# Kernel tuning notes

Measured on AMD Instinct MI355X. Metric: run time of the kernel, lower is better.

The kernel has to match this reference:

```python
import jax, jax.numpy as jnp
import numpy as np

EPS = 1e-6      # zero-token detection eps
LN_EPS = 1e-5   # torch LayerNorm default
H = 8           # num_heads


def setup_inputs() -> dict:
    key = jax.random.key(0)
    ks = jax.random.split(key, 6)
    B, T, D = 4, 2048, 512
    embs = jax.random.normal(ks[0], (B, T, D), jnp.float32)
    labels = jax.random.uniform(ks[1], (B, T), jnp.float32)
    s = 1.0 / np.sqrt(D)
    ln_g = jnp.ones((D,), jnp.float32)
    ln_b = jnp.zeros((D,), jnp.float32)
    in_proj_w = jax.random.uniform(ks[2], (3 * D, D), jnp.float32, -s, s)
    in_proj_b = jnp.zeros((3 * D,), jnp.float32)
    out_w = jax.random.uniform(ks[3], (D, D), jnp.float32, -s, s)
    out_b = jnp.zeros((D,), jnp.float32)
    alpha = jnp.float32(1.0)
    beta = jnp.float32(0.0)
    return {"embs": embs, "labels": labels, "ln_g": ln_g, "ln_b": ln_b,
            "in_proj_w": in_proj_w, "in_proj_b": in_proj_b,
            "out_w": out_w, "out_b": out_b, "alpha": alpha, "beta": beta}


def reference(embs, labels, ln_g, ln_b, in_proj_w, in_proj_b, out_w, out_b, alpha, beta):
    B, T, D = embs.shape
    h, dh = H, D // H
    # pre-LayerNorm
    mu = embs.mean(-1, keepdims=True)
    var = ((embs - mu) ** 2).mean(-1, keepdims=True)
    x = (embs - mu) / jnp.sqrt(var + LN_EPS) * ln_g + ln_b
    # key padding mask from all-zero tokens (computed on normalized x, as in source)
    kpm = jnp.abs(x).sum(-1) <= EPS                      # [B,T] bool
    w = jnp.where(kpm, jnp.float32(0.0), labels)         # zero labels on masked tokens
    # fused qkv projection (nn.MultiheadAttention in_proj)
    qkv = x @ in_proj_w.T + in_proj_b                    # [B,T,3D]
    q, k, v = jnp.split(qkv, 3, axis=-1)
    def sp(a):
        return a.reshape(B, T, h, dh).transpose(0, 2, 1, 3)  # [B,h,T,dh]
    q, k, v = sp(q), sp(k), sp(v)
    scores = jnp.einsum('bhqd,bhkd->bhqk', q, k) / np.sqrt(dh)
    # additive label bias: alpha * labels (broadcast over heads & queries) + beta
    scores = scores + (alpha * w[:, None, None, :] + beta)
    # key padding mask -> -inf (use large negative for stability)
    scores = jnp.where(kpm[:, None, None, :], jnp.float32(-1e30), scores)
    a = jax.nn.softmax(scores, axis=-1)
    o = jnp.einsum('bhqk,bhkd->bhqd', a, v).transpose(0, 2, 1, 3).reshape(B, T, D)
    o = o @ out_w.T + out_b
    o = jnp.nan_to_num(o, nan=0.0, posinf=0.0, neginf=0.0)
    # masked mean pool over T
    m = (~kpm)[..., None].astype(o.dtype)                # [B,T,1]
    pooled = (o * m).sum(1) / jnp.maximum(m.sum(1), 1.0)  # [B,D]
    return pooled
```

## Files before the change

kernel.cpp:

```cpp
#include <hip/hip_runtime.h>
#include <math.h>

#define T 2048
#define D 512
#define NH 8
#define DH 64
#define NB 4
#define NTOK (NB * T)
#define LOG2E 1.44269504f
#define QSCALE (0.125f * LOG2E)

using bf16x8 = __attribute__((ext_vector_type(8))) short;
using f32x4  = __attribute__((ext_vector_type(4))) float;

static __device__ __forceinline__ unsigned short f2bf(float f) {
    union { float f; unsigned u; } v; v.f = f;
    unsigned r = v.u + 0x7fffu + ((v.u >> 16) & 1u);
    return (unsigned short)(r >> 16);
}
#if __has_builtin(__builtin_amdgcn_cvt_pk_bf16_f32)
static __device__ __forceinline__ unsigned pack_bf16_pair(float a, float b) {
    auto r = __builtin_amdgcn_cvt_pk_bf16_f32(a, b);
    union { decltype(r) v; unsigned u; } c; c.v = r;
    return c.u;
}
#else
static __device__ __forceinline__ unsigned pack_bf16_pair(float a, float b) {
    union { float f; unsigned u; } ua, ub; ua.f = a; ub.f = b;
    unsigned ra = ua.u + 0x7fffu + ((ua.u >> 16) & 1u);
    unsigned rb = ub.u + 0x7fffu + ((ub.u >> 16) & 1u);
    return __builtin_amdgcn_perm(rb, ra, 0x07060302);
}
#endif


__global__ __launch_bounds__(256) void ln_kernel(
    const float* __restrict__ embs, const float* __restrict__ labels,
    const float* __restrict__ g, const float* __restrict__ bb,
    const float* __restrict__ alpha_p, const float* __restrict__ beta_p,
    unsigned short* __restrict__ xfrag, float* __restrict__ wexp,
    float* __restrict__ kpmf)
{
    __shared__ __align__(16) unsigned short Xs[16][520];
    int tid = threadIdx.x, wave = tid >> 6, lane = tid & 63;
    int quad = lane >> 4, lm = lane & 15;
    int t16 = blockIdx.x;

    float4 g0 = *(const float4*)(g + lane * 8), g1 = *(const float4*)(g + lane * 8 + 4);
    float4 c0 = *(const float4*)(bb + lane * 8), c1 = *(const float4*)(bb + lane * 8 + 4);
    float gv[8] = {g0.x, g0.y, g0.z, g0.w, g1.x, g1.y, g1.z, g1.w};
    float cv[8] = {c0.x, c0.y, c0.z, c0.w, c1.x, c1.y, c1.z, c1.w};

    for (int tt = 0; tt < 4; ++tt) {
        int n = t16 * 16 + wave * 4 + tt;
        const float* e = embs + (size_t)n * D + lane * 8;
        float4 a4 = *(const float4*)e, b4 = *(const float4*)(e + 4);
        float v[8] = {a4.x, a4.y, a4.z, a4.w, b4.x, b4.y, b4.z, b4.w};

        float s = 0.f, ss = 0.f;
        #pragma unroll
        for (int j = 0; j < 8; ++j) { s += v[j]; ss += v[j] * v[j]; }
        #pragma unroll
        for (int o = 1; o <= 32; o <<= 1) {
            s += __shfl_xor(s, o, 64);
            ss += __shfl_xor(ss, o, 64);
        }
        float mu = s * (1.0f / D);
        float var = ss * (1.0f / D) - mu * mu;
        float rstd = rsqrtf(var + 1e-5f);

        float x[8], as = 0.f;
        #pragma unroll
        for (int j = 0; j < 8; ++j) {
            x[j] = (v[j] - mu) * rstd * gv[j] + cv[j];
            as += fabsf(x[j]);
        }
        uint4 pk;
        pk.x = pack_bf16_pair(x[0], x[1]);
        pk.y = pack_bf16_pair(x[2], x[3]);
        pk.z = pack_bf16_pair(x[4], x[5]);
        pk.w = pack_bf16_pair(x[6], x[7]);
        *(uint4*)&Xs[wave * 4 + tt][lane * 8] = pk;

        #pragma unroll
        for (int o = 1; o <= 32; o <<= 1) as += __shfl_xor(as, o, 64);
        if (lane == 0) {
            int kpm = (as <= 1e-6f);
            kpmf[n] = kpm ? 1.0f : 0.0f;
            wexp[n] = kpm ? 0.0f : __expf(alpha_p[0] * labels[n] + beta_p[0]);
        }
    }
    __syncthreads();
    #pragma unroll
    for (int i = 0; i < 4; ++i) {
        int kc = wave * 4 + i;
        bf16x8 fr = *(const bf16x8*)&Xs[lm][kc * 32 + quad * 8];
        *(bf16x8*)(xfrag + ((size_t)(t16 * 16 + kc) * 64 + lane) * 8) = fr;
    }
}

__global__ __launch_bounds__(256) void wconv_kernel(
    const float* __restrict__ w, unsigned short* __restrict__ wbfrag)
{
    __shared__ __align__(16) unsigned short Ws[16][520];
    int tid = threadIdx.x, wave = tid >> 6, lane = tid & 63;
    int quad = lane >> 4, lm = lane & 15;
    int j16 = blockIdx.x;

    for (int tt = 0; tt < 4; ++tt) {
        int j = j16 * 16 + wave * 4 + tt;
        const float* wp = w + (size_t)j * D + lane * 8;
        float4 a4 = *(const float4*)wp, b4 = *(const float4*)(wp + 4);
        uint4 pk;
        pk.x = pack_bf16_pair(a4.x, a4.y);
        pk.y = pack_bf16_pair(a4.z, a4.w);
        pk.z = pack_bf16_pair(b4.x, b4.y);
        pk.w = pack_bf16_pair(b4.z, b4.w);
        *(uint4*)&Ws[wave * 4 + tt][lane * 8] = pk;
    }
    __syncthreads();
    #pragma unroll
    for (int i = 0; i < 4; ++i) {
        int kc = wave * 4 + i;
        bf16x8 fr = *(const bf16x8*)&Ws[lm][kc * 32 + quad * 8];
        *(bf16x8*)(wbfrag + ((size_t)(j16 * 16 + kc) * 64 + lane) * 8) = fr;
    }
}

__global__ __launch_bounds__(256) void wfrag_fill(
    const float* __restrict__ wexp, unsigned short* __restrict__ vfrag)
{
    int idx = blockIdx.x * 256 + threadIdx.x;
    int lane = idx & 63, chunk = idx >> 6;
    int kk = chunk & 1, t64 = (chunk >> 1) & 31, bh = chunk >> 6;
    int lm = lane & 15, quad = lane >> 4;
    int b_ = bh >> 3;
    size_t base = (((size_t)chunk * 5 + 4) * 64 + lane) * 8;
    if (lm == 0) {
        int key0 = t64 * 64 + kk * 32 + quad * 8;
        const float* wp = wexp + b_ * T + key0;
        unsigned short vv[8];
        #pragma unroll
        for (int e = 0; e < 8; ++e) vv[e] = f2bf(wp[e]);
        *(uint4*)(vfrag + base) = *(uint4*)vv;
    } else {
        uint4 z = {0u, 0u, 0u, 0u};
        *(uint4*)(vfrag + base) = z;
    }
}

__global__ __launch_bounds__(256) void qkv_mfma(
    const unsigned short* __restrict__ xfrag, const unsigned short* __restrict__ wbfrag,
    const float* __restrict__ bias, const float* __restrict__ wexp,
    unsigned short* __restrict__ qfrag, unsigned short* __restrict__ kfrag,
    unsigned short* __restrict__ vfrag)
{
    __shared__ __align__(16) unsigned short Ls[4][64][72];
    int tid = threadIdx.x;
    int wave = tid >> 6, lane = tid & 63, quad = lane >> 4, lm = lane & 15;
    int wr = wave >> 1, wc = wave & 1;
    int m0 = blockIdx.x * 128 + wr * 64;
    int j0 = blockIdx.y * 128 + wc * 64;
    int mt16 = m0 >> 4, jt16 = j0 >> 4;

    f32x4 acc[4][4];
    #pragma unroll
    for (int a = 0; a < 4; ++a)
        #pragma unroll
        for (int b = 0; b < 4; ++b) acc[a][b] = (f32x4){0.f,0.f,0.f,0.f};

    bf16x8 af0[4], bf0[4], af1[4], bf1[4];
    auto load_ab = [&](int kc, bf16x8 (&af)[4], bf16x8 (&bf)[4]) {
        #pragma unroll
        for (int mf = 0; mf < 4; ++mf)
            af[mf] = *(const bf16x8*)(xfrag + ((size_t)((mt16 + mf) * 16 + kc) * 64 + lane) * 8);
        #pragma unroll
        for (int nt = 0; nt < 4; ++nt)
            bf[nt] = *(const bf16x8*)(wbfrag + ((size_t)((jt16 + nt) * 16 + kc) * 64 + lane) * 8);
    };
    auto do_mfma = [&](bf16x8 (&af)[4], bf16x8 (&bf)[4]) {
        #pragma unroll
        for (int mf = 0; mf < 4; ++mf)
            #pragma unroll
            for (int nt = 0; nt < 4; ++nt)
                acc[mf][nt] = __builtin_amdgcn_mfma_f32_16x16x32_bf16(af[mf], bf[nt], acc[mf][nt], 0, 0, 0);
    };

    load_ab(0, af0, bf0);
    for (int kc = 0; kc < 16; kc += 2) {
        load_ab(kc + 1, af1, bf1);
        do_mfma(af0, bf0);
        load_ab((kc + 2) & 15, af0, bf0);
        do_mfma(af1, bf1);
    }

    int part = j0 >> 9;
    int h = (j0 & 511) >> 6;
    int b_ = m0 >> 11, tloc = m0 & (T - 1);
    int bh = b_ * NH + h;
    float bcol[4];
    #pragma unroll
    for (int nt = 0; nt < 4; ++nt) bcol[nt] = bias[j0 + nt * 16 + lm];

    if (part == 2) {
        float wv[4][4];
        #pragma unroll
        for (int mf = 0; mf < 4; ++mf)
            #pragma unroll
            for (int r = 0; r < 4; ++r)
                wv[mf][r] = wexp[b_ * T + tloc + mf * 16 + quad * 4 + r];
        #pragma unroll
        for (int mf = 0; mf < 4; ++mf)
            #pragma unroll
            for (int nt = 0; nt < 4; ++nt) {
                uint2 pw;
                pw.x = pack_bf16_pair((acc[mf][nt][0] + bcol[nt]) * wv[mf][0],
                                      (acc[mf][nt][1] + bcol[nt]) * wv[mf][1]);
                pw.y = pack_bf16_pair((acc[mf][nt][2] + bcol[nt]) * wv[mf][2],
                                      (acc[mf][nt][3] + bcol[nt]) * wv[mf][3]);
                *(uint2*)&Ls[wave][nt * 16 + lm][mf * 16 + quad * 4] = pw;
            }
        #pragma unroll
        for (int nt = 0; nt < 4; ++nt)
            #pragma unroll
            for (int kk = 0; kk < 2; ++kk) {
                bf16x8 fr = *(const bf16x8*)&Ls[wave][nt * 16 + lm][kk * 32 + quad * 8];
                size_t chunk = ((((size_t)bh * 32 + (tloc >> 6)) * 2 + kk) * 5) + nt;
                *(bf16x8*)(vfrag + chunk * 512 + lane * 8) = fr;
            }
    } else {
        float scale = (part == 0) ? QSCALE : 1.0f;
        #pragma unroll
        for (int mf = 0; mf < 4; ++mf)
            #pragma unroll
            for (int nt = 0; nt < 4; ++nt)
                #pragma unroll
                for (int r = 0; r < 4; ++r)
                    Ls[wave][mf * 16 + quad * 4 + r][nt * 16 + lm] =
                        f2bf((acc[mf][nt][r] + bcol[nt]) * scale);
        if (part == 0) {
            #pragma unroll
            for (int mf = 0; mf < 4; ++mf)
                #pragma unroll
                for (int kk = 0; kk < 2; ++kk) {
                    bf16x8 fr = *(const bf16x8*)&Ls[wave][mf * 16 + lm][kk * 32 + quad * 8];
                    size_t chunk = ((size_t)bh * 128 + (tloc >> 4) + mf) * 2 + kk;
                    *(bf16x8*)(qfrag + chunk * 512 + lane * 8) = fr;
                }
        } else {
            #pragma unroll
            for (int nta = 0; nta < 4; ++nta)
                #pragma unroll
                for (int kk = 0; kk < 2; ++kk) {
                    bf16x8 fr = *(const bf16x8*)&Ls[wave][lm * 4 + nta][kk * 32 + quad * 8];
                    size_t chunk = ((((size_t)bh * 32 + (tloc >> 6)) * 2 + kk) * 4) + nta;
                    *(bf16x8*)(kfrag + chunk * 512 + lane * 8) = fr;
                }
        }
    }
}

__global__ __launch_bounds__(256, 2) void attn_mfma(
    const unsigned short* __restrict__ qfrag, const unsigned short* __restrict__ kfrag,
    const unsigned short* __restrict__ vfrag, const float* __restrict__ kpmf,
    float* __restrict__ S)
{
    __shared__ __align__(16) unsigned short Ps[4][64][72];
    __shared__ float Lx[2][2][64];
    int g = blockIdx.x;
    int bh = g & 31, q0 = (g >> 5) * 128;
    int tid = threadIdx.x, wave = tid >> 6, lane = tid & 63;
    int quad = lane >> 4, lm = lane & 15;
    int qh = wave >> 1, ks = wave & 1;
    int qbase = q0 + qh * 64;
    int b_ = bh >> 3, h = bh & 7;

    bf16x8 qf[4][2];
    int t16b = (qbase >> 4);
    #pragma unroll
    for (int mf = 0; mf < 4; ++mf)
        #pragma unroll
        for (int kk = 0; kk < 2; ++kk)
            qf[mf][kk] = *(const bf16x8*)(qfrag +
                (((size_t)(bh * 128 + t16b + mf) * 2 + kk) * 64 + lane) * 8);

    f32x4 accO[4][4], accL[4];
    #pragma unroll
    for (int mf = 0; mf < 4; ++mf) {
        #pragma unroll
        for (int nt = 0; nt < 4; ++nt) accO[mf][nt] = (f32x4){0.f,0.f,0.f,0.f};
        accL[mf] = (f32x4){0.f,0.f,0.f,0.f};
    }

    const unsigned short* kb = kfrag + (size_t)bh * 32 * 8 * 512 + (size_t)lane * 8;
    const unsigned short* vb = vfrag + (size_t)bh * 32 * 10 * 512 + (size_t)lane * 8;
    int t0k = ks * 16;

    bf16x8 kf0[4][2], kf1[4][2];
    auto load_k = [&](int t64, bf16x8 (&kf)[4][2]) {
        const unsigned short* p = kb + (size_t)t64 * 8 * 512;
        #pragma unroll
        for (int kk = 0; kk < 2; ++kk)
            #pragma unroll
            for (int nt = 0; nt < 4; ++nt)
                kf[nt][kk] = *(const bf16x8*)(p + ((size_t)kk * 4 + nt) * 512);
    };

    auto process = [&](int t64, bf16x8 (&kf)[4][2]) {
        const unsigned short* p = vb + (size_t)t64 * 10 * 512;
        bf16x8 vf[5][2];
        #pragma unroll
        for (int kk = 0; kk < 2; ++kk)
            #pragma unroll
            for (int nt = 0; nt < 5; ++nt)
                vf[nt][kk] = *(const bf16x8*)(p + ((size_t)kk * 5 + nt) * 512);

        #pragma unroll
        for (int mf = 0; mf < 4; ++mf) {
            f32x4 s[4];
            #pragma unroll
            for (int nt = 0; nt < 4; ++nt) {
                f32x4 t0 = (f32x4){0.f,0.f,0.f,0.f};
                t0 = __builtin_amdgcn_mfma_f32_16x16x32_bf16(qf[mf][0], kf[nt][0], t0, 0, 0, 0);
                t0 = __builtin_amdgcn_mfma_f32_16x16x32_bf16(qf[mf][1], kf[nt][1], t0, 0, 0, 0);
                s[nt] = t0;
            }
            int rowb = mf * 16 + quad * 4;
            #pragma unroll
            for (int r = 0; r < 4; ++r) {
                float p0 = __builtin_amdgcn_exp2f(s[0][r]);
                float p1 = __builtin_amdgcn_exp2f(s[1][r]);
                float p2 = __builtin_amdgcn_exp2f(s[2][r]);
                float p3 = __builtin_amdgcn_exp2f(s[3][r]);
                uint2 pw;
                pw.x = pack_bf16_pair(p0, p1);
                pw.y = pack_bf16_pair(p2, p3);
                *(uint2*)&Ps[wave][rowb + r][lm * 4] = pw;
            }
        }

        bf16x8 pf[4][2];
        #pragma unroll
        for (int mf = 0; mf < 4; ++mf)
            #pragma unroll
            for (int kk = 0; kk < 2; ++kk)
                pf[mf][kk] = *(const bf16x8*)&Ps[wave][mf * 16 + lm][kk * 32 + quad * 8];

        #pragma unroll
        for (int mf = 0; mf < 4; ++mf) {
            #pragma unroll
            for (int nt = 0; nt < 4; ++nt) {
                accO[mf][nt] = __builtin_amdgcn_mfma_f32_16x16x32_bf16(pf[mf][0], vf[nt][0], accO[mf][nt], 0, 0, 0);
                accO[mf][nt] = __builtin_amdgcn_mfma_f32_16x16x32_bf16(pf[mf][1], vf[nt][1], accO[mf][nt], 0, 0, 0);
            }
            accL[mf] = __builtin_amdgcn_mfma_f32_16x16x32_bf16(pf[mf][0], vf[4][0], accL[mf], 0, 0, 0);
            accL[mf] = __builtin_amdgcn_mfma_f32_16x16x32_bf16(pf[mf][1], vf[4][1], accL[mf], 0, 0, 0);
        }
    };

    load_k(t0k, kf0);
    for (int i = 0; i < 16; i += 2) {
        load_k(t0k + i + 1, kf1);
        process(t0k + i, kf0);
        load_k(t0k + ((i + 2) & 15), kf0);
        process(t0k + i + 1, kf1);
    }

    if (lm == 0) {
        #pragma unroll
        for (int mf = 0; mf < 4; ++mf)
            #pragma unroll
            for (int r = 0; r < 4; ++r)
                Lx[qh][ks][mf * 16 + quad * 4 + r] = accL[mf][r];
    }
    __syncthreads();

    float pooled[4] = {0.f, 0.f, 0.f, 0.f};
    #pragma unroll
    for (int mf = 0; mf < 4; ++mf)
        #pragma unroll
        for (int r = 0; r < 4; ++r) {
            int rloc = mf * 16 + quad * 4 + r;
            float l = Lx[qh][0][rloc] + Lx[qh][1][rloc];
            float w = (1.0f - kpmf[b_ * T + qbase + rloc]) / l;
            #pragma unroll
            for (int nt = 0; nt < 4; ++nt) pooled[nt] += accO[mf][nt][r] * w;
        }
    #pragma unroll
    for (int nt = 0; nt < 4; ++nt) {
        pooled[nt] += __shfl_xor(pooled[nt], 16, 64);
        pooled[nt] += __shfl_xor(pooled[nt], 32, 64);
    }
    if (quad == 0) {
        #pragma unroll
        for (int nt = 0; nt < 4; ++nt)
            atomicAdd(&S[b_ * D + h * DH + nt * 16 + lm], pooled[nt]);
    }
}

__global__ __launch_bounds__(256) void out_kernel(
    const float* __restrict__ S, const float* __restrict__ kpmf,
    const float* __restrict__ Wo, const float* __restrict__ bo,
    float* __restrict__ out)
{
    __shared__ float Sl[512];
    __shared__ float cs[4];
    __shared__ float pr[4][64];
    int b_ = blockIdx.x >> 3;
    int cg = blockIdx.x & 7;
    int tid = threadIdx.x;
    int col = tid & 63, kq = tid >> 6;
    Sl[tid] = S[b_ * D + tid];
    Sl[tid + 256] = S[b_ * D + tid + 256];
    const float* kp = kpmf + b_ * T;
    float c = 0.f;
    for (int t = tid; t < T; t += 256) c += kp[t];
    #pragma unroll
    for (int o = 32; o; o >>= 1) c += __shfl_xor(c, o, 64);
    if ((tid & 63) == 0) cs[tid >> 6] = c;
    __syncthreads();
    float masked = cs[0] + cs[1] + cs[2] + cs[3];
    float cnt = (float)T - masked;
    float inv = 1.0f / fmaxf(cnt, 1.0f);

    int d = cg * 64 + col;
    const float4* wr4 = (const float4*)(Wo + (size_t)d * D + kq * 128);
    float dot = 0.f;
    #pragma unroll 8
    for (int i = 0; i < 32; ++i) {
        float4 w4 = wr4[i];
        int kbase = kq * 128 + i * 4;
        dot += Sl[kbase + 0] * w4.x + Sl[kbase + 1] * w4.y +
               Sl[kbase + 2] * w4.z + Sl[kbase + 3] * w4.w;
    }
    pr[kq][col] = dot;
    __syncthreads();
    if (kq == 0) {
        float tot = pr[0][col] + pr[1][col] + pr[2][col] + pr[3][col];
        out[b_ * D + d] = (tot + bo[d] * cnt) * inv;
    }
}

extern "C" void kernel_launch(void* const* d_in, const int* in_sizes, int n_in,
                              void* d_out, int out_size, void* d_ws, size_t ws_size,
                              hipStream_t stream) {
    const float* embs   = (const float*)d_in[0];
    const float* labels = (const float*)d_in[1];
    const float* ln_g   = (const float*)d_in[2];
    const float* ln_b   = (const float*)d_in[3];
    const float* ipw    = (const float*)d_in[4];
    const float* ipb    = (const float*)d_in[5];
    const float* ow     = (const float*)d_in[6];
    const float* obb    = (const float*)d_in[7];
    const float* alpha  = (const float*)d_in[8];
    const float* beta   = (const float*)d_in[9];
    float* out = (float*)d_out;

    unsigned short* xfrag  = (unsigned short*)d_ws;
    unsigned short* wbfrag = xfrag + (size_t)NTOK * D;
    unsigned short* qfrag  = wbfrag + (size_t)3 * D * D;
    unsigned short* kfrag  = qfrag + (size_t)NTOK * D;
    unsigned short* vfrag  = kfrag + (size_t)NTOK * D;
    float* wexp = (float*)(vfrag + (size_t)32 * 32 * 2 * 5 * 512);
    float* kpmf = wexp + NTOK;
    float* S    = kpmf + NTOK;

    hipMemsetAsync(S, 0, (size_t)NB * D * sizeof(float), stream);
    ln_kernel<<<NTOK / 16, 256, 0, stream>>>(embs, labels, ln_g, ln_b, alpha, beta,
                                             xfrag, wexp, kpmf);
    wconv_kernel<<<(3 * D) / 16, 256, 0, stream>>>(ipw, wbfrag);
    wfrag_fill<<<512, 256, 0, stream>>>(wexp, vfrag);
    dim3 gq(NTOK / 128, (3 * D) / 128);
    qkv_mfma<<<gq, 256, 0, stream>>>(xfrag, wbfrag, ipb, wexp, qfrag, kfrag, vfrag);
    attn_mfma<<<32 * (T / 128), 256, 0, stream>>>(qfrag, kfrag, vfrag, kpmf, S);
    out_kernel<<<NB * 8, 256, 0, stream>>>(S, kpmf, ow, obb, out);
}
```

Measured before the change: 165.3 us.

## Software-pipeline QK-exp and PV stages with double-buffered P tiles

Restructures the attention inner loop so the QK^T+exp2 stage for key tile t runs alongside the PV MFMA stage for tile t-1. P tiles now go through a double-buffered LDS array, and the K register double buffer is replaced by a single buffer that is loaded ahead. s_setprio raises wave priority around the MFMA sections so MFMA work can interleave with exp/LDS work from other waves. The goal is to hide LDS round-trip and transcendental latency behind matrix work. The cost is double the LDS for P and possible register-pressure changes, which could hurt occupancy at 2 blocks per CU.

```diff
diff --git a/kernel.cpp b/kernel.cpp
--- a/kernel.cpp
+++ b/kernel.cpp
@@ -265,7 +265,7 @@
     const unsigned short* __restrict__ vfrag, const float* __restrict__ kpmf,
     float* __restrict__ S)
 {
-    __shared__ __align__(16) unsigned short Ps[4][64][72];
+    __shared__ __align__(16) unsigned short Ps[4][2][64][72];
     __shared__ float Lx[2][2][64];
     int g = blockIdx.x;
     int bh = g & 31, q0 = (g >> 5) * 128;
@@ -296,8 +296,8 @@
     const unsigned short* vb = vfrag + (size_t)bh * 32 * 10 * 512 + (size_t)lane * 8;
     int t0k = ks * 16;
 
-    bf16x8 kf0[4][2], kf1[4][2];
-    auto load_k = [&](int t64, bf16x8 (&kf)[4][2]) {
+    bf16x8 kf[4][2];
+    auto load_k = [&](int t64) {
         const unsigned short* p = kb + (size_t)t64 * 8 * 512;
         #pragma unroll
         for (int kk = 0; kk < 2; ++kk)
@@ -305,19 +305,26 @@
             for (int nt = 0; nt < 4; ++nt)
                 kf[nt][kk] = *(const bf16x8*)(p + ((size_t)kk * 4 + nt) * 512);
     };
-
-    auto process = [&](int t64, bf16x8 (&kf)[4][2]) {
+    auto load_v = [&](int t64, bf16x8 (&vf)[5][2]) {
         const unsigned short* p = vb + (size_t)t64 * 10 * 512;
-        bf16x8 vf[5][2];
         #pragma unroll
         for (int kk = 0; kk < 2; ++kk)
             #pragma unroll
             for (int nt = 0; nt < 5; ++nt)
                 vf[nt][kk] = *(const bf16x8*)(p + ((size_t)kk * 5 + nt) * 512);
-
+    };
+    auto load_p = [&](int buf, bf16x8 (&pf)[4][2]) {
+        #pragma unroll
+        for (int mf = 0; mf < 4; ++mf)
+            #pragma unroll
+            for (int kk = 0; kk < 2; ++kk)
+                pf[mf][kk] = *(const bf16x8*)&Ps[wave][buf][mf * 16 + lm][kk * 32 + quad * 8];
+    };
+    auto qk_exp = [&](int buf) {
         #pragma unroll
         for (int mf = 0; mf < 4; ++mf) {
             f32x4 s[4];
+            __builtin_amdgcn_s_setprio(1);
             #pragma unroll
             for (int nt = 0; nt < 4; ++nt) {
                 f32x4 t0 = (f32x4){0.f,0.f,0.f,0.f};
@@ -325,6 +332,7 @@
                 t0 = __builtin_amdgcn_mfma_f32_16x16x32_bf16(qf[mf][1], kf[nt][1], t0, 0, 0, 0);
                 s[nt] = t0;
             }
+            __builtin_amdgcn_s_setprio(0);
             int rowb = mf * 16 + quad * 4;
             #pragma unroll
             for (int r = 0; r < 4; ++r) {
@@ -335,17 +343,12 @@
                 uint2 pw;
                 pw.x = pack_bf16_pair(p0, p1);
                 pw.y = pack_bf16_pair(p2, p3);
-                *(uint2*)&Ps[wave][rowb + r][lm * 4] = pw;
+                *(uint2*)&Ps[wave][buf][rowb + r][lm * 4] = pw;
             }
         }
-
-        bf16x8 pf[4][2];
-        #pragma unroll
-        for (int mf = 0; mf < 4; ++mf)
-            #pragma unroll
-            for (int kk = 0; kk < 2; ++kk)
-                pf[mf][kk] = *(const bf16x8*)&Ps[wave][mf * 16 + lm][kk * 32 + quad * 8];
-
+    };
+    auto pv = [&](bf16x8 (&pf)[4][2], bf16x8 (&vf)[5][2]) {
+        __builtin_amdgcn_s_setprio(1);
         #pragma unroll
         for (int mf = 0; mf < 4; ++mf) {
             #pragma unroll
@@ -356,14 +359,25 @@
             accL[mf] = __builtin_amdgcn_mfma_f32_16x16x32_bf16(pf[mf][0], vf[4][0], accL[mf], 0, 0, 0);
             accL[mf] = __builtin_amdgcn_mfma_f32_16x16x32_bf16(pf[mf][1], vf[4][1], accL[mf], 0, 0, 0);
         }
-    };
-
-    load_k(t0k, kf0);
-    for (int i = 0; i < 16; i += 2) {
-        load_k(t0k + i + 1, kf1);
-        process(t0k + i, kf0);
-        load_k(t0k + ((i + 2) & 15), kf0);
-        process(t0k + i + 1, kf1);
+        __builtin_amdgcn_s_setprio(0);
+    };
+
+    load_k(t0k);
+    qk_exp(0);
+    load_k(t0k + 1);
+    for (int t = 1; t < 16; ++t) {
+        bf16x8 pf[4][2], vf[5][2];
+        load_p((t - 1) & 1, pf);
+        load_v(t0k + t - 1, vf);
+        qk_exp(t & 1);
+        load_k(t0k + ((t + 1) & 15));
+        pv(pf, vf);
+    }
+    {
+        bf16x8 pf[4][2], vf[5][2];
+        load_p(1, pf);
+        load_v(t0k + 15, vf);
+        pv(pf, vf);
     }
 
     if (lm == 0) {
```

Result: faster. 157.2 us (-4.9%).
